# Optimization experiments

Measured on AMD Instinct MI355X. Metric: run time of the kernel, lower is better.

## Reference

```python
import jax, jax.numpy as jnp
import numpy as np

def _dct_mat():
    k = np.arange(8)[:, None]
    n = np.arange(8)[None, :]
    norm = np.where(k == 0, np.sqrt(1.0 / 8.0), np.sqrt(2.0 / 8.0))
    return jnp.asarray(norm * np.cos(np.pi / 8.0 * (n + 0.5) * k), jnp.float32)

_LUM = np.array([[16,11,10,16,24,40,51,61],[12,12,14,19,26,58,60,55],[14,13,16,24,40,57,69,56],[14,17,22,29,51,87,80,62],[18,22,37,56,68,109,103,77],[24,35,55,64,81,104,113,92],[49,64,78,87,103,121,120,101],[72,92,95,98,112,100,103,99]], np.float32)
_CHROM = np.array([[17,18,24,47,99,99,99,99],[18,21,26,66,99,99,99,99],[24,26,56,99,99,99,99,99],[47,66,99,99,99,99,99,99],[99,99,99,99,99,99,99,99],[99,99,99,99,99,99,99,99],[99,99,99,99,99,99,99,99],[99,99,99,99,99,99,99,99]], np.float32)

def _qtables(quality):
    q = max(1, min(100, int(quality)))
    scale = 5000.0 / q if q < 50 else 200.0 - 2.0 * q
    tbs = np.stack([_LUM, _CHROM]) * scale
    tbs = np.clip((tbs + 50.0) / 100.0, 1.0, 255.0)
    return jnp.asarray(tbs, jnp.float32)

def _jpeg_forward(img, quality):
    bs, _, oh, ow = img.shape
    x = img * 255.0
    pad_h = (8 - oh % 8) % 8
    pad_w = (8 - ow % 8) % 8
    if pad_h or pad_w:
        x = jnp.pad(x, ((0, 0), (0, 0), (0, pad_h), (0, pad_w)), mode='edge')
    h, w = oh + pad_h, ow + pad_w
    W_ycc = jnp.asarray([[0.299, 0.587, 0.114], [-0.1687, -0.3313, 0.5], [0.5, -0.4187, -0.0813]], jnp.float32)
    b_ycc = jnp.asarray([0.0, 128.0, 128.0], jnp.float32)
    # 1x1 conv colorspace transform
    yuv = jnp.einsum('oc,bchw->bohw', W_ycc, x) + b_ycc[None, :, None, None]
    nb = bs * 3
    hb, wb = h // 8, w // 8
    # unfold(kernel=8, stride=8) == non-overlapping 8x8 blocking, block-row-major
    blocks = yuv.reshape(nb, hb, 8, wb, 8).transpose(0, 1, 3, 2, 4).reshape(nb, hb * wb, 8, 8)
    M = _dct_mat()
    dct = jnp.matmul(M, jnp.matmul(blocks - 128.0, M.T))
    qt = _qtables(quality)
    # faithful to original slicing patches_dct[:bs] / [bs:] over the flattened (b,c) dim
    row = jnp.arange(nb)[:, None, None, None]
    qfull = jnp.where(row < bs, qt[0], qt[1])
    t = dct / qfull
    # straight-through round
    tq = (t + jax.lax.stop_gradient(jnp.round(t) - t)) * qfull
    idct = jnp.matmul(M.T, jnp.matmul(tq, M)) + 128.0
    rec = idct.reshape(nb, hb, wb, 8, 8).transpose(0, 1, 3, 2, 4).reshape(bs, 3, h, w)
    rec = rec - b_ycc[None, :, None, None]
    y, cb, cr = rec[:, 0], rec[:, 1], rec[:, 2]
    r = y + 1.402 * cr
    g = y - 0.34414 * cb - 0.71414 * cr
    b = y + 1.772 * cb
    rgb = jnp.stack([r, g, b], axis=1)[:, :, :oh, :ow]
    return jnp.clip(rgb / 255.0, 0.0, 1.0)

def setup_inputs() -> dict:
    key = jax.random.key(0)
    img = jax.random.uniform(key, (16, 3, 512, 512), dtype=jnp.float32)
    return {"img": img, "quality": 80}

def reference(img, quality):
    return _jpeg_forward(img, quality)
```

## Files before the change

kernel.cpp:

```cpp
#include <hip/hip_runtime.h>
#include <math.h>

#define C1 0.9807852804032304
#define C2 0.9238795325112867
#define C3 0.8314696123025452
#define C4 0.7071067811865476
#define C5 0.5555702330196022
#define C6 0.3826834323650898
#define C7 0.19509032201612825
#define N0 0.35355339059327373

static constexpr double Mc[8][8] = {
 {  N0,      N0,      N0,      N0,      N0,      N0,      N0,      N0    },
 {  .5*C1,   .5*C3,   .5*C5,   .5*C7,  -.5*C7,  -.5*C5,  -.5*C3,  -.5*C1 },
 {  .5*C2,   .5*C6,  -.5*C6,  -.5*C2,  -.5*C2,  -.5*C6,   .5*C6,   .5*C2 },
 {  .5*C3,  -.5*C7,  -.5*C1,  -.5*C5,   .5*C5,   .5*C1,   .5*C7,  -.5*C3 },
 {  .5*C4,  -.5*C4,  -.5*C4,   .5*C4,   .5*C4,  -.5*C4,  -.5*C4,   .5*C4 },
 {  .5*C5,  -.5*C1,   .5*C7,   .5*C3,  -.5*C3,  -.5*C7,   .5*C1,  -.5*C5 },
 {  .5*C6,  -.5*C2,   .5*C2,  -.5*C6,  -.5*C6,   .5*C2,  -.5*C2,   .5*C6 },
 {  .5*C7,  -.5*C5,   .5*C3,  -.5*C1,   .5*C1,  -.5*C3,   .5*C5,  -.5*C7 },
};
#define ROWF(r) {(float)Mc[r][0],(float)Mc[r][1],(float)Mc[r][2],(float)Mc[r][3],\
                 (float)Mc[r][4],(float)Mc[r][5],(float)Mc[r][6],(float)Mc[r][7]}
static constexpr float Mcf[8][8] = {ROWF(0),ROWF(1),ROWF(2),ROWF(3),ROWF(4),ROWF(5),ROWF(6),ROWF(7)};

static __device__ const double LUM_BASE[64] = {
 16,11,10,16,24,40,51,61,
 12,12,14,19,26,58,60,55,
 14,13,16,24,40,57,69,56,
 14,17,22,29,51,87,80,62,
 18,22,37,56,68,109,103,77,
 24,35,55,64,81,104,113,92,
 49,64,78,87,103,121,120,101,
 72,92,95,98,112,100,103,99};
static __device__ const double CHROM_BASE[64] = {
 17,18,24,47,99,99,99,99,
 18,21,26,66,99,99,99,99,
 24,26,56,99,99,99,99,99,
 47,66,99,99,99,99,99,99,
 99,99,99,99,99,99,99,99,
 99,99,99,99,99,99,99,99,
 99,99,99,99,99,99,99,99,
 99,99,99,99,99,99,99,99};

__global__ __launch_bounds__(192, 2) void jpeg_fwd(const float* __restrict__ img,
                                                   const int* __restrict__ quality,
                                                   float* __restrict__ out)
{
    __shared__ double QT[128];
    __shared__ double U[1728];
    double* TR1 = U;
    float*  TR2 = (float*)U;
    float*  RECf = (float*)U + 1728;

    const int t   = threadIdx.x;
    const int w   = t >> 6;
    const int l   = t & 63;
    const int blk = l >> 3;
    const int rr  = l & 7;

    const int b    = blockIdx.x >> 9;
    const int rem  = blockIdx.x & 511;
    const int row0 = (rem >> 3) << 3;
    const int col0 = (rem & 7) << 6;

    const size_t plane = 512 * 512;

    const float* p = img + (size_t)(b * 3) * plane + (size_t)(row0 + rr) * 512 + col0 + blk * 8;
    float4 R0 = *(const float4*)(p);
    float4 R1 = *(const float4*)(p + 4);
    float4 G0 = *(const float4*)(p + plane);
    float4 G1 = *(const float4*)(p + plane + 4);
    float4 B0 = *(const float4*)(p + 2 * plane);
    float4 B1 = *(const float4*)(p + 2 * plane + 4);

    if (t < 128) {
        int tbl = t >> 6, e = t & 63;
        int q   = quality[0];
        q = q < 1 ? 1 : (q > 100 ? 100 : q);
        double scale = (q < 50) ? (5000.0 / (double)q) : (200.0 - 2.0 * (double)q);
        double base  = tbl ? CHROM_BASE[e] : LUM_BASE[e];
        double v = (base * scale + 50.0) / 100.0;
        QT[t] = fmin(fmax(v, 1.0), 255.0);
    }
    __syncthreads();

    const double W00 =  0.299,   W01 =  0.587,   W02 =  0.114;
    const double W10 = -0.1687,  W11 = -0.3313,  W12 =  0.5;
    const double W20 =  0.5,     W21 = -0.4187,  W22 = -0.0813;

    float rf[8] = {R0.x, R0.y, R0.z, R0.w, R1.x, R1.y, R1.z, R1.w};
    float gf[8] = {G0.x, G0.y, G0.z, G0.w, G1.x, G1.y, G1.z, G1.w};
    float bf[8] = {B0.x, B0.y, B0.z, B0.w, B1.x, B1.y, B1.z, B1.w};

    double row[8];
    #pragma unroll
    for (int k = 0; k < 8; ++k) {
        double rv = (double)rf[k] * 255.0;
        double gv = (double)gf[k] * 255.0;
        double bv = (double)bf[k] * 255.0;
        double v;
        if (w == 0)      v = W00 * rv + W01 * gv + W02 * bv;
        else if (w == 1) v = W10 * rv + W11 * gv + W12 * bv + 128.0;
        else             v = W20 * rv + W21 * gv + W22 * bv + 128.0;
        row[k] = v - 128.0;
    }

    double y[8];
    #pragma unroll
    for (int c = 0; c < 8; ++c) {
        double s = 0.0;
        #pragma unroll
        for (int k = 0; k < 8; ++k)
            s += row[k] * Mc[c][k];
        y[c] = s;
    }

    {
        double* tb = TR1 + w * 576 + blk * 72 + rr * 9;
        #pragma unroll
        for (int k = 0; k < 8; ++k) tb[k] = y[k];
    }
    __syncthreads();
    double t1[8], qv[8];
    {
        const double* tb = TR1 + w * 576 + blk * 72 + rr;
        #pragma unroll
        for (int k = 0; k < 8; ++k) t1[k] = tb[k * 9];
    }
    const int sel = ((b * 3 + w) < 16) ? 0 : 1;
    #pragma unroll
    for (int j = 0; j < 8; ++j) qv[j] = QT[(sel << 6) + (j << 3) + rr];

    double wq[8];
    #pragma unroll
    for (int j = 0; j < 8; ++j) {
        double s = 0.0;
        #pragma unroll
        for (int k = 0; k < 8; ++k)
            s += t1[k] * Mc[j][k];
        wq[j] = rint(s / qv[j]) * qv[j];
    }

    float wqf[8];
    #pragma unroll
    for (int k = 0; k < 8; ++k) wqf[k] = (float)wq[k];

    float a3[8];
    #pragma unroll
    for (int j = 0; j < 8; ++j) {
        float s = 0.0f;
        #pragma unroll
        for (int k = 0; k < 8; ++k)
            s += wqf[k] * Mcf[k][j];
        a3[j] = s;
    }

    __syncthreads();
    {
        float* tb = TR2 + w * 576 + blk * 72 + rr * 9;
        #pragma unroll
        for (int k = 0; k < 8; ++k) tb[k] = a3[k];
    }
    __syncthreads();
    float t2[8];
    {
        const float* tb = TR2 + w * 576 + blk * 72 + rr;
        #pragma unroll
        for (int k = 0; k < 8; ++k) t2[k] = tb[k * 9];
    }

    {
        float o[8];
        #pragma unroll
        for (int i = 0; i < 8; ++i) {
            float s = 0.0f;
            #pragma unroll
            for (int k = 0; k < 8; ++k)
                s += t2[k] * Mcf[k][i];
            o[i] = s + 128.0f;
        }
        float* rc = RECf + w * 544 + rr * 68 + blk * 8;
        *(float4*)(rc)     = make_float4(o[0], o[1], o[2], o[3]);
        *(float4*)(rc + 4) = make_float4(o[4], o[5], o[6], o[7]);
    }
    __syncthreads();

    const float* rY = RECf + 0 * 544 + rr * 68 + blk * 8;
    const float* rU = RECf + 1 * 544 + rr * 68 + blk * 8;
    const float* rV = RECf + 2 * 544 + rr * 68 + blk * 8;
    float4 Y0 = *(const float4*)(rY);
    float4 Y1 = *(const float4*)(rY + 4);
    float4 U0 = *(const float4*)(rU);
    float4 U1 = *(const float4*)(rU + 4);
    float4 V0 = *(const float4*)(rV);
    float4 V1 = *(const float4*)(rV + 4);
    float yv[8] = {Y0.x, Y0.y, Y0.z, Y0.w, Y1.x, Y1.y, Y1.z, Y1.w};
    float uv[8] = {U0.x, U0.y, U0.z, U0.w, U1.x, U1.y, U1.z, U1.w};
    float vv[8] = {V0.x, V0.y, V0.z, V0.w, V1.x, V1.y, V1.z, V1.w};

    float* q0 = out + (size_t)(b * 3 + w) * plane + (size_t)(row0 + rr) * 512 + col0 + blk * 8;
    float o[8];
    #pragma unroll
    for (int k = 0; k < 8; ++k) {
        float yd = yv[k];
        float cb = uv[k] - 128.0f;
        float cr = vv[k] - 128.0f;
        float v;
        if (w == 0)      v = yd + 1.402f * cr;
        else if (w == 1) v = yd - 0.34414f * cb - 0.71414f * cr;
        else             v = yd + 1.772f * cb;
        o[k] = fminf(fmaxf(v * (1.0f / 255.0f), 0.0f), 1.0f);
    }
    *(float4*)(q0)     = make_float4(o[0], o[1], o[2], o[3]);
    *(float4*)(q0 + 4) = make_float4(o[4], o[5], o[6], o[7]);
}

extern "C" void kernel_launch(void* const* d_in, const int* in_sizes, int n_in,
                              void* d_out, int out_size, void* d_ws, size_t ws_size,
                              hipStream_t stream) {
    const float* img     = (const float*)d_in[0];
    const int*   quality = (const int*)d_in[1];
    float*       out     = (float*)d_out;
    jpeg_fwd<<<8192, 192, 0, stream>>>(img, quality, out);
}
```

Baseline: 114.4 us.

## Fuse final IDCT with color conversion per thread, drop shared recon stage

Each thread reads all three channels' transposed intermediates and computes their final inverse DCT pass itself, then converts to RGB directly. This removes the reconstruction shared-memory round trip and one block barrier, at the cost of three times the arithmetic in that stage. The launch bound's minimum blocks per CU is raised to push for higher occupancy, which constrains registers and may cause spills.

New measurement: 115.4 us. No clear change (+0.8%).

```diff
diff --git a/kernel.cpp b/kernel.cpp
--- a/kernel.cpp
+++ b/kernel.cpp
@@ -43,7 +43,7 @@
  99,99,99,99,99,99,99,99,
  99,99,99,99,99,99,99,99};
 
-__global__ __launch_bounds__(192, 2) void jpeg_fwd(const float* __restrict__ img,
+__global__ __launch_bounds__(192, 4) void jpeg_fwd(const float* __restrict__ img,
                                                    const int* __restrict__ quality,
                                                    float* __restrict__ out)
 {
@@ -51,7 +51,6 @@
     __shared__ double U[1728];
     double* TR1 = U;
     float*  TR2 = (float*)U;
-    float*  RECf = (float*)U + 1728;
 
     const int t   = threadIdx.x;
     const int w   = t >> 6;
@@ -163,53 +162,42 @@
         for (int k = 0; k < 8; ++k) tb[k] = a3[k];
     }
     __syncthreads();
-    float t2[8];
-    {
-        const float* tb = TR2 + w * 576 + blk * 72 + rr;
-        #pragma unroll
-        for (int k = 0; k < 8; ++k) t2[k] = tb[k * 9];
-    }
-
-    {
-        float o[8];
-        #pragma unroll
-        for (int i = 0; i < 8; ++i) {
-            float s = 0.0f;
-            #pragma unroll
-            for (int k = 0; k < 8; ++k)
-                s += t2[k] * Mcf[k][i];
-            o[i] = s + 128.0f;
+
+    float tY[8], tU[8], tV[8];
+    {
+        const float* t0 = TR2 + 0 * 576 + blk * 72 + rr;
+        const float* u0 = TR2 + 1 * 576 + blk * 72 + rr;
+        const float* v0 = TR2 + 2 * 576 + blk * 72 + rr;
+        #pragma unroll
+        for (int k = 0; k < 8; ++k) {
+            tY[k] = t0[k * 9];
+            tU[k] = u0[k * 9];
+            tV[k] = v0[k * 9];
         }
-        float* rc = RECf + w * 544 + rr * 68 + blk * 8;
-        *(float4*)(rc)     = make_float4(o[0], o[1], o[2], o[3]);
-        *(float4*)(rc + 4) = make_float4(o[4], o[5], o[6], o[7]);
-    }
-    __syncthreads();
-
-    const float* rY = RECf + 0 * 544 + rr * 68 + blk * 8;
-    const float* rU = RECf + 1 * 544 + rr * 68 + blk * 8;
-    const float* rV = RECf + 2 * 544 + rr * 68 + blk * 8;
-    float4 Y0 = *(const float4*)(rY);
-    float4 Y1 = *(const float4*)(rY + 4);
-    float4 U0 = *(const float4*)(rU);
-    float4 U1 = *(const float4*)(rU + 4);
-    float4 V0 = *(const float4*)(rV);
-    float4 V1 = *(const float4*)(rV + 4);
-    float yv[8] = {Y0.x, Y0.y, Y0.z, Y0.w, Y1.x, Y1.y, Y1.z, Y1.w};
-    float uv[8] = {U0.x, U0.y, U0.z, U0.w, U1.x, U1.y, U1.z, U1.w};
-    float vv[8] = {V0.x, V0.y, V0.z, V0.w, V1.x, V1.y, V1.z, V1.w};
+    }
+
+    float yr[8], ur[8], vr[8];
+    #pragma unroll
+    for (int j = 0; j < 8; ++j) {
+        float sy = 0.0f, su = 0.0f, sv = 0.0f;
+        #pragma unroll
+        for (int k = 0; k < 8; ++k) {
+            sy += tY[k] * Mcf[k][j];
+            su += tU[k] * Mcf[k][j];
+            sv += tV[k] * Mcf[k][j];
+        }
+        yr[j] = sy; ur[j] = su; vr[j] = sv;
+    }
 
     float* q0 = out + (size_t)(b * 3 + w) * plane + (size_t)(row0 + rr) * 512 + col0 + blk * 8;
     float o[8];
     #pragma unroll
     for (int k = 0; k < 8; ++k) {
-        float yd = yv[k];
-        float cb = uv[k] - 128.0f;
-        float cr = vv[k] - 128.0f;
+        float yd = yr[k] + 128.0f;
         float v;
-        if (w == 0)      v = yd + 1.402f * cr;
-        else if (w == 1) v = yd - 0.34414f * cb - 0.71414f * cr;
-        else             v = yd + 1.772f * cb;
+        if (w == 0)      v = yd + 1.402f * vr[k];
+        else if (w == 1) v = yd - 0.34414f * ur[k] - 0.71414f * vr[k];
+        else             v = yd + 1.772f * ur[k];
         o[k] = fminf(fmaxf(v * (1.0f / 255.0f), 0.0f), 1.0f);
     }
     *(float4*)(q0)     = make_float4(o[0], o[1], o[2], o[3]);
```
